# Performance work log

Hardware: AMD Instinct MI355X
Metric: run time of the kernel (lower is better)

The kernel has to match this reference:

```python
import jax, jax.numpy as jnp
import numpy as np

B, S, C, H = 2, 2048, 1024, 16
D = C // H  # depth per head = 64


def mish(x):
    return x * jnp.tanh(jax.nn.softplus(x))


def setup_inputs() -> dict:
    key = jax.random.key(0)
    ks = jax.random.split(key, 11)
    s = 1.0 / np.sqrt(C)
    return {
        "x": jax.random.normal(ks[0], (B, S, C), jnp.float32),
        "y": jax.random.normal(ks[1], (B, S, C), jnp.float32),
        "t_mat": jax.random.normal(ks[2], (B, S, S), jnp.float32),
        "wq": jax.random.normal(ks[3], (C, C), jnp.float32) * s,
        "bq": jnp.zeros((C,), jnp.float32),
        "wk": jax.random.normal(ks[4], (C, C), jnp.float32) * s,
        "bk": jnp.zeros((C,), jnp.float32),
        "wv": jax.random.normal(ks[5], (C, C), jnp.float32) * s,
        "bv": jnp.zeros((C,), jnp.float32),
        "wc": jax.random.normal(ks[6], (H,), jnp.float32),   # 1x1 Conv2D, 1 in-channel -> H out-channels
        "bc": jnp.zeros((H,), jnp.float32),
        "wf": jax.random.normal(ks[7], (C, C), jnp.float32) * s,  # 1x1 Conv1D == per-position Dense
        "bf": jnp.zeros((C,), jnp.float32),
    }


def _split_heads(t):
    # (B, S, C) -> (B*H, S, D)
    return t.reshape(B, S, H, D).transpose(0, 2, 1, 3).reshape(B * H, S, D)


def reference(x, y, t_mat, wq, bq, wk, bk, wv, bv, wc, bc, wf, bf):
    q = _split_heads(y @ wq + bq)   # (BH, S, D)
    k = _split_heads(x @ wk + bk)
    v = _split_heads(y @ wv + bv)

    # context: 1x1 conv + tanh over t_mat -> (B, S, S, H) -> (B*H, S, S)
    c = jnp.tanh(t_mat[..., None] * wc + bc)
    c = c.transpose(0, 3, 1, 2).reshape(B * H, S, S)

    qk = jnp.einsum("bkd,bqd->bkq", k, q) / jnp.sqrt(jnp.float32(D))  # (BH, Sk, Sq)
    cv = jnp.einsum("bks,bsd->bkd", c, v)                             # (BH, S, D)
    att = jnp.einsum("bkq,bqd->bkd", qk, cv)                          # (BH, S, D)

    # merge heads: (BH, S, D) -> (B, S, C)
    merged = att.reshape(B, H, S, D).transpose(0, 2, 1, 3).reshape(B, S, C)
    return mish(merged @ wf + bf)
```

## Files before the change

### kernel.cpp

```cpp
#include <hip/hip_runtime.h>
#include <math.h>

#define B_ 2
#define S_ 2048
#define C_ 1024
#define H_ 16
#define D_ 64

typedef __bf16 bf16_t;
typedef __attribute__((ext_vector_type(8))) __bf16 bf16x8;
typedef __attribute__((ext_vector_type(4))) __bf16 bf16x4;
typedef __attribute__((ext_vector_type(4))) float f32x4;

__device__ __forceinline__ void gload16(const void* g, void* l) {
    __builtin_amdgcn_global_load_lds(
        (const __attribute__((address_space(1))) unsigned int*)g,
        (__attribute__((address_space(3))) unsigned int*)l, 16, 0, 0);
}

__device__ __forceinline__ float tanh_fast(float z) {
    z = fminf(fmaxf(z, -12.f), 12.f);
    float e = __expf(2.f * z);
    return 1.f - __fdividef(2.f, e + 1.f);
}

__device__ __forceinline__ float mish_f(float x) {
    float sp = (x > 15.f) ? x : log1pf(__expf(x));
    return x * tanh_fast(sp);
}

__device__ __forceinline__ float tanh_folded(float t, float w2, float b2) {
    float e = __builtin_amdgcn_exp2f(fmaf(t, w2, b2));
    float r = __builtin_amdgcn_rcpf(e + 1.f);
    return fmaf(-2.f, r, 1.f);
}

__global__ __launch_bounds__(256) void prep_kernel(
    const float* __restrict__ y, bf16_t* __restrict__ ybf,
    const float* __restrict__ x, bf16_t* __restrict__ xbf,
    const float* __restrict__ wq, const float* __restrict__ wk,
    const float* __restrict__ wv,
    bf16_t* __restrict__ wqt, bf16_t* __restrict__ wkt,
    bf16_t* __restrict__ wvt)
{
    __shared__ float ts[64][65];
    const int bid = blockIdx.x;
    const int t = threadIdx.x;
    if (bid < 4096) {
        const float* in = (bid < 2048) ? y : x;
        bf16_t* out = (bid < 2048) ? ybf : xbf;
        size_t i = ((size_t)(bid & 2047) * 256 + t) * 8;
        float4 u = *(const float4*)&in[i];
        float4 v = *(const float4*)&in[i + 4];
        bf16x8 o;
        o[0] = (bf16_t)u.x; o[1] = (bf16_t)u.y; o[2] = (bf16_t)u.z; o[3] = (bf16_t)u.w;
        o[4] = (bf16_t)v.x; o[5] = (bf16_t)v.y; o[6] = (bf16_t)v.z; o[7] = (bf16_t)v.w;
        *(bf16x8*)&out[i] = o;
    } else {
        const int r3 = bid - 4096;
        const int z = r3 >> 8;
        const int rem = r3 & 255;
        const int k0 = (rem >> 4) * 64, n0 = (rem & 15) * 64;
        const float* in = z == 0 ? wq : (z == 1 ? wk : wv);
        bf16_t* out = z == 0 ? wqt : (z == 1 ? wkt : wvt);
        const int r = t >> 2, c0 = (t & 3) * 16;
        #pragma unroll
        for (int j = 0; j < 16; j += 4) {
            float4 v = *(const float4*)&in[(size_t)(k0 + r) * C_ + n0 + c0 + j];
            ts[c0 + j + 0][r] = v.x; ts[c0 + j + 1][r] = v.y;
            ts[c0 + j + 2][r] = v.z; ts[c0 + j + 3][r] = v.w;
        }
        __syncthreads();
        #pragma unroll
        for (int g = 0; g < 2; ++g) {
            bf16x8 o;
            #pragma unroll
            for (int e = 0; e < 8; ++e) o[e] = (bf16_t)ts[r][c0 + g * 8 + e];
            *(bf16x8*)&out[(size_t)(n0 + r) * C_ + k0 + c0 + g * 8] = o;
        }
    }
}

__global__ __launch_bounds__(256) void qkv_proj(
    const bf16_t* __restrict__ ybf, const bf16_t* __restrict__ xbf,
    const bf16_t* __restrict__ wqt, const bf16_t* __restrict__ wkt,
    const bf16_t* __restrict__ wvt,
    const float* __restrict__ bq, const float* __restrict__ bk,
    const float* __restrict__ bv,
    bf16_t* __restrict__ Qt, bf16_t* __restrict__ Kb, bf16_t* __restrict__ Vt)
{
    const int z = blockIdx.z;
    const bf16_t* A  = (z == 1) ? xbf : ybf;
    const bf16_t* Bt = (z == 0) ? wqt : (z == 1) ? wkt : wvt;
    const float* bias = (z == 0) ? bq : (z == 1) ? bk : bv;
    const int K = C_;

    __shared__ bf16_t As[128 * 32];
    __shared__ bf16_t Bs[128 * 32];

    const int t = threadIdx.x;
    const int w = t >> 6, lane = t & 63;
    const int wm = (w >> 1) * 64, wn = (w & 1) * 64;
    const int l15 = lane & 15, l4 = lane >> 4;
    const int row0 = blockIdx.y * 128, col0 = blockIdx.x * 128;

    const int sr = t >> 2, sk = (t & 3) * 8;
    const bf16_t* gA = A + (size_t)(row0 + sr) * K + sk;
    const bf16_t* gB = Bt + (size_t)(col0 + sr) * K + sk;
    bf16_t* lA = As + (t & ~63) * 8;
    bf16_t* lB = Bs + (t & ~63) * 8;

    f32x4 acc[4][4] = {};

    for (int k0 = 0; k0 < K; k0 += 32) {
        __syncthreads();
        gload16(gA + k0, lA);
        gload16(gA + k0 + (size_t)64 * K, lA + 2048);
        gload16(gB + k0, lB);
        gload16(gB + k0 + (size_t)64 * K, lB + 2048);
        __syncthreads();
        bf16x8 a[4], b[4];
        #pragma unroll
        for (int i = 0; i < 4; ++i)
            a[i] = *(const bf16x8*)&As[(wm + i * 16 + l15) * 32 + l4 * 8];
        #pragma unroll
        for (int j = 0; j < 4; ++j)
            b[j] = *(const bf16x8*)&Bs[(wn + j * 16 + l15) * 32 + l4 * 8];
        #pragma unroll
        for (int i = 0; i < 4; ++i)
            #pragma unroll
            for (int j = 0; j < 4; ++j)
                acc[i][j] = __builtin_amdgcn_mfma_f32_16x16x32_bf16(
                    a[i], b[j], acc[i][j], 0, 0, 0);
    }

    if (z != 1) {
        bf16_t* To = (z == 0) ? Qt : Vt;
        #pragma unroll
        for (int i = 0; i < 4; ++i) {
            int mb = row0 + wm + i * 16 + l4 * 4;
            int b2 = mb >> 11, s = mb & 2047;
            #pragma unroll
            for (int j = 0; j < 4; ++j) {
                int c = col0 + wn + j * 16 + l15;
                float bv2 = bias[c];
                bf16x4 o;
                #pragma unroll
                for (int r = 0; r < 4; ++r) o[r] = (bf16_t)(acc[i][j][r] + bv2);
                *(bf16x4*)&To[((size_t)b2 * C_ + c) * S_ + s] = o;
            }
        }
    } else {
        #pragma unroll
        for (int i = 0; i < 4; ++i)
            #pragma unroll
            for (int j = 0; j < 4; ++j) {
                int c = col0 + wn + j * 16 + l15;
                float bv2 = bias[c];
                #pragma unroll
                for (int r = 0; r < 4; ++r) {
                    int m = row0 + wm + i * 16 + l4 * 4 + r;
                    Kb[(size_t)m * C_ + c] = (bf16_t)(acc[i][j][r] + bv2);
                }
            }
    }
}

__global__ __launch_bounds__(256) void cv_qtcv_fused(
    const float* __restrict__ t_mat, const bf16_t* __restrict__ Vt,
    const bf16_t* __restrict__ Qt,
    const float* __restrict__ wc, const float* __restrict__ bc,
    float* __restrict__ Mm)
{
    const int bh = blockIdx.z, b = bh >> 4, h = bh & 15;
    const int q0 = blockIdx.x * 128;
    const int p = blockIdx.y;
    const int t = threadIdx.x;
    const int w = t >> 6, lane = t & 63;
    const int l15 = lane & 15, l4 = lane >> 4;

    __shared__ bf16_t smem[10240];
    bf16_t* As = smem;
    bf16_t* Bs = smem + 4096;
    bf16_t* cvs = smem;

    const float LOG2E2 = 2.8853900817779268f;
    const float wch2 = wc[h] * LOG2E2, bch2 = bc[h] * LOG2E2;
    const float* tb = t_mat + (size_t)b * S_ * S_ + (size_t)q0 * S_;
    const bf16_t* Vb = Vt + ((size_t)b * C_ + h * 64) * S_;

    const int rr = t >> 1, sp = (t & 1) * 16;
    const int vd = t >> 2, vse = (t & 3) * 8;
    const int lBoff = (t & ~63) * 8;

    f32x4 acc[2][4] = {};

    const int s_beg = p * 512, s_end = s_beg + 512;
    const float* trow = tb + (size_t)rr * S_ + sp;

    float4 v0 = *(const float4*)&trow[s_beg];
    float4 v1 = *(const float4*)&trow[s_beg + 4];
    float4 v2 = *(const float4*)&trow[s_beg + 8];
    float4 v3 = *(const float4*)&trow[s_beg + 12];

    int buf = 0;
    for (int s0 = s_beg; s0 < s_end; s0 += 32, buf ^= 1) {
        bf16x8 p0, p1;
        p0[0] = (bf16_t)tanh_folded(v0.x, wch2, bch2);
        p0[1] = (bf16_t)tanh_folded(v0.y, wch2, bch2);
        p0[2] = (bf16_t)tanh_folded(v0.z, wch2, bch2);
        p0[3] = (bf16_t)tanh_folded(v0.w, wch2, bch2);
        p0[4] = (bf16_t)tanh_folded(v1.x, wch2, bch2);
        p0[5] = (bf16_t)tanh_folded(v1.y, wch2, bch2);
        p0[6] = (bf16_t)tanh_folded(v1.z, wch2, bch2);
        p0[7] = (bf16_t)tanh_folded(v1.w, wch2, bch2);
        p1[0] = (bf16_t)tanh_folded(v2.x, wch2, bch2);
        p1[1] = (bf16_t)tanh_folded(v2.y, wch2, bch2);
        p1[2] = (bf16_t)tanh_folded(v2.z, wch2, bch2);
        p1[3] = (bf16_t)tanh_folded(v2.w, wch2, bch2);
        p1[4] = (bf16_t)tanh_folded(v3.x, wch2, bch2);
        p1[5] = (bf16_t)tanh_folded(v3.y, wch2, bch2);
        p1[6] = (bf16_t)tanh_folded(v3.z, wch2, bch2);
        p1[7] = (bf16_t)tanh_folded(v3.w, wch2, bch2);
        gload16(Vb + (size_t)vd * S_ + s0 + vse, Bs + buf * 2048 + lBoff);
        *(bf16x8*)&As[rr * 32 + sp] = p0;
        *(bf16x8*)&As[rr * 32 + sp + 8] = p1;
        __syncthreads();
        if (s0 + 32 < s_end) {
            const float* nrow = &trow[s0 + 32];
            v0 = *(const float4*)&nrow[0];
            v1 = *(const float4*)&nrow[4];
            v2 = *(const float4*)&nrow[8];
            v3 = *(const float4*)&nrow[12];
        }
        bf16x8 a0 = *(const bf16x8*)&As[(w * 32 + l15) * 32 + l4 * 8];
        bf16x8 a1 = *(const bf16x8*)&As[(w * 32 + 16 + l15) * 32 + l4 * 8];
        #pragma unroll
        for (int j = 0; j < 4; ++j) {
            bf16x8 bb = *(const bf16x8*)&Bs[buf * 2048 + (j * 16 + l15) * 32 + l4 * 8];
            acc[0][j] = __builtin_amdgcn_mfma_f32_16x16x32_bf16(a0, bb, acc[0][j], 0, 0, 0);
            acc[1][j] = __builtin_amdgcn_mfma_f32_16x16x32_bf16(a1, bb, acc[1][j], 0, 0, 0);
        }
    }

    __syncthreads();
    #pragma unroll
    for (int i = 0; i < 2; ++i)
        #pragma unroll
        for (int j = 0; j < 4; ++j) {
            int d = j * 16 + l15;
            bf16x4 o;
            #pragma unroll
            for (int r = 0; r < 4; ++r) o[r] = (bf16_t)acc[i][j][r];
            *(bf16x4*)&cvs[(size_t)w * 2560 + d * 40 + i * 16 + l4 * 4] = o;
        }
    __syncthreads();

    const bf16_t* Qrow = Qt + ((size_t)b * C_ + h * 64 + w * 16 + l15) * S_ + q0 + l4 * 8;
    f32x4 macc[4] = {};
    #pragma unroll
    for (int c = 0; c < 4; ++c) {
        bf16x8 a = *(const bf16x8*)&Qrow[c * 32];
        #pragma unroll
        for (int j = 0; j < 4; ++j) {
            bf16x8 bb = *(const bf16x8*)&cvs[(size_t)c * 2560 + (j * 16 + l15) * 40 + l4 * 8];
            macc[j] = __builtin_amdgcn_mfma_f32_16x16x32_bf16(a, bb, macc[j], 0, 0, 0);
        }
    }

    float* mp = Mm + (size_t)bh * 64 * 64;
    #pragma unroll
    for (int j = 0; j < 4; ++j)
        #pragma unroll
        for (int r = 0; r < 4; ++r)
            atomicAdd(&mp[(size_t)(w * 16 + l4 * 4 + r) * 64 + j * 16 + l15],
                      macc[j][r]);
}

__global__ __launch_bounds__(256) void weff_kernel(
    const float* __restrict__ Mm, const float* __restrict__ wf,
    bf16_t* __restrict__ Wefft)
{
    const int b = blockIdx.z, h = blockIdx.y;
    const int co0 = blockIdx.x * 64;
    const int t = threadIdx.x;
    const int tx = t & 15, ty = t >> 4;

    __shared__ float Ms[64][64];
    __shared__ float Ws[64][64];

    const float* Mb = Mm + (size_t)(b * H_ + h) * 64 * 64;

    const int r  = t >> 2;
    const int c4 = (t & 3) << 2;

    #pragma unroll
    for (int rep = 0; rep < 4; ++rep) {
        int col = c4 + rep * 16;
        float4 m4 = *(const float4*)&Mb[(size_t)r * 64 + col];
        Ms[col + 0][r] = m4.x; Ms[col + 1][r] = m4.y;
        Ms[col + 2][r] = m4.z; Ms[col + 3][r] = m4.w;
        float4 w4 = *(const float4*)&wf[(size_t)(h * 64 + r) * C_ + co0 + col];
        *(float4*)&Ws[r][col] = w4;
    }
    __syncthreads();

    float acc[4][4] = {};
    #pragma unroll
    for (int kk = 0; kk < 64; ++kk) {
        float av[4], bv2[4];
        *(float4*)&av[0] = *(const float4*)&Ms[kk][ty * 4];
        *(float4*)&bv2[0] = *(const float4*)&Ws[kk][tx * 4];
        #pragma unroll
        for (int i = 0; i < 4; ++i)
            #pragma unroll
            for (int j = 0; j < 4; ++j)
                acc[i][j] = fmaf(av[i], bv2[j], acc[i][j]);
    }

    bf16_t* wp = Wefft + (size_t)b * C_ * C_;
    #pragma unroll
    for (int i = 0; i < 4; ++i)
        #pragma unroll
        for (int j = 0; j < 4; ++j)
            wp[(size_t)(co0 + tx * 4 + j) * C_ + h * 64 + ty * 4 + i] =
                (bf16_t)(acc[i][j] * 0.125f);
}

__global__ __launch_bounds__(256) void final_gemm(
    const bf16_t* __restrict__ Kb, const bf16_t* __restrict__ Weft,
    const float* __restrict__ bias, float* __restrict__ out)
{
    const int z = blockIdx.z;
    const bf16_t* A  = Kb + (size_t)z * S_ * C_;
    const bf16_t* Bt = Weft + (size_t)z * C_ * C_;
    float* Co = out + (size_t)z * S_ * C_;
    const int K = C_;

    __shared__ bf16_t As[128 * 32];
    __shared__ bf16_t Bs[64 * 32];

    const int t = threadIdx.x;
    const int w = t >> 6, lane = t & 63;
    const int l15 = lane & 15, l4 = lane >> 4;
    const int row0 = blockIdx.y * 128, col0 = blockIdx.x * 64;

    const int sr = t >> 2, sk = (t & 3) * 8;
    const bf16_t* gA = A + (size_t)(row0 + sr) * K + sk;
    const bf16_t* gB = Bt + (size_t)(col0 + sr) * K + sk;
    bf16_t* lA = As + (t & ~63) * 8;
    bf16_t* lB = Bs + (t & ~63) * 8;

    f32x4 acc[2][4] = {};

    for (int k0 = 0; k0 < K; k0 += 32) {
        __syncthreads();
        gload16(gA + k0, lA);
        gload16(gA + k0 + (size_t)64 * K, lA + 2048);
        gload16(gB + k0, lB);
        __syncthreads();
        bf16x8 a0 = *(const bf16x8*)&As[(w * 32 + l15) * 32 + l4 * 8];
        bf16x8 a1 = *(const bf16x8*)&As[(w * 32 + 16 + l15) * 32 + l4 * 8];
        #pragma unroll
        for (int j = 0; j < 4; ++j) {
            bf16x8 bb = *(const bf16x8*)&Bs[(j * 16 + l15) * 32 + l4 * 8];
            acc[0][j] = __builtin_amdgcn_mfma_f32_16x16x32_bf16(a0, bb, acc[0][j], 0, 0, 0);
            acc[1][j] = __builtin_amdgcn_mfma_f32_16x16x32_bf16(a1, bb, acc[1][j], 0, 0, 0);
        }
    }

    #pragma unroll
    for (int i = 0; i < 2; ++i)
        #pragma unroll
        for (int j = 0; j < 4; ++j) {
            int c = col0 + j * 16 + l15;
            float bv2 = bias[c];
            #pragma unroll
            for (int r = 0; r < 4; ++r) {
                int m = row0 + w * 32 + i * 16 + l4 * 4 + r;
                Co[(size_t)m * C_ + c] = mish_f(acc[i][j][r] + bv2);
            }
        }
}

extern "C" void kernel_launch(void* const* d_in, const int* in_sizes, int n_in,
                              void* d_out, int out_size, void* d_ws, size_t ws_size,
                              hipStream_t stream) {
    const float* x     = (const float*)d_in[0];
    const float* y     = (const float*)d_in[1];
    const float* t_mat = (const float*)d_in[2];
    const float* wq    = (const float*)d_in[3];
    const float* bq    = (const float*)d_in[4];
    const float* wk    = (const float*)d_in[5];
    const float* bk    = (const float*)d_in[6];
    const float* wv    = (const float*)d_in[7];
    const float* bv    = (const float*)d_in[8];
    const float* wc    = (const float*)d_in[9];
    const float* bc    = (const float*)d_in[10];
    const float* wf    = (const float*)d_in[11];
    const float* bf    = (const float*)d_in[12];
    float* out = (float*)d_out;

    char* base = (char*)d_ws;
    bf16_t* Qt   = (bf16_t*)(base + 0);
    bf16_t* Kb   = (bf16_t*)(base + 8388608);
    bf16_t* Vt   = (bf16_t*)(base + 16777216);
    float*  Mm   = (float*) (base + 25165824);
    bf16_t* Weft = (bf16_t*)(base + 25690112);
    bf16_t* ybf  = (bf16_t*)(base + 29884416);
    bf16_t* xbf  = (bf16_t*)(base + 38273024);
    bf16_t* wqt  = (bf16_t*)(base + 46661632);
    bf16_t* wkt  = (bf16_t*)(base + 48758784);
    bf16_t* wvt  = (bf16_t*)(base + 50855936);

    hipMemsetAsync(Mm, 0, (size_t)B_ * H_ * 64 * 64 * sizeof(float), stream);

    dim3 blk(256);

    prep_kernel<<<dim3(4864), blk, 0, stream>>>(
        y, ybf, x, xbf, wq, wk, wv, wqt, wkt, wvt);

    qkv_proj<<<dim3(C_ / 128, (B_ * S_) / 128, 3), blk, 0, stream>>>(
        ybf, xbf, wqt, wkt, wvt, bq, bk, bv, Qt, Kb, Vt);

    cv_qtcv_fused<<<dim3(S_ / 128, 4, B_ * H_), blk, 0, stream>>>(
        t_mat, Vt, Qt, wc, bc, Mm);

    weff_kernel<<<dim3(C_ / 64, H_, B_), blk, 0, stream>>>(Mm, wf, Weft);

    final_gemm<<<dim3(C_ / 64, S_ / 128, B_), blk, 0, stream>>>(
        Kb, Weft, bf, out);
}
```

Baseline: 274.1 us.

## Process two heads per block in fused cv kernel to reuse t_mat loads

Each block of the fused context-value kernel now handles a pair of heads, so every t_mat tile loaded from global memory feeds two tanh transforms and two MFMA accumulations. This halves the t_mat reads, which dominate memory traffic (t_mat is read once per head). In exchange there is twice the accumulator registers, more LDS (32KB), half as many blocks, and the Q·cv epilogue runs serially for both heads.

```diff
diff --git a/kernel.cpp b/kernel.cpp
--- a/kernel.cpp
+++ b/kernel.cpp
@@ -33,6 +33,19 @@
     float e = __builtin_amdgcn_exp2f(fmaf(t, w2, b2));
     float r = __builtin_amdgcn_rcpf(e + 1.f);
     return fmaf(-2.f, r, 1.f);
+}
+
+__device__ __forceinline__ bf16x8 tanh8(float4 u, float4 v, float w2, float b2) {
+    bf16x8 o;
+    o[0] = (bf16_t)tanh_folded(u.x, w2, b2);
+    o[1] = (bf16_t)tanh_folded(u.y, w2, b2);
+    o[2] = (bf16_t)tanh_folded(u.z, w2, b2);
+    o[3] = (bf16_t)tanh_folded(u.w, w2, b2);
+    o[4] = (bf16_t)tanh_folded(v.x, w2, b2);
+    o[5] = (bf16_t)tanh_folded(v.y, w2, b2);
+    o[6] = (bf16_t)tanh_folded(v.z, w2, b2);
+    o[7] = (bf16_t)tanh_folded(v.w, w2, b2);
+    return o;
 }
 
 __global__ __launch_bounds__(256) void prep_kernel(
@@ -172,28 +185,34 @@
     const float* __restrict__ wc, const float* __restrict__ bc,
     float* __restrict__ Mm)
 {
-    const int bh = blockIdx.z, b = bh >> 4, h = bh & 15;
+    const int bhp = blockIdx.z;
+    const int b = bhp >> 3, hp = bhp & 7;
+    const int h0 = hp * 2, h1 = h0 + 1;
     const int q0 = blockIdx.x * 128;
     const int p = blockIdx.y;
     const int t = threadIdx.x;
     const int w = t >> 6, lane = t & 63;
     const int l15 = lane & 15, l4 = lane >> 4;
 
-    __shared__ bf16_t smem[10240];
-    bf16_t* As = smem;
-    bf16_t* Bs = smem + 4096;
+    __shared__ bf16_t smem[16384];
+    bf16_t* As0 = smem;
+    bf16_t* As1 = smem + 4096;
+    bf16_t* Bsb = smem + 8192;
     bf16_t* cvs = smem;
 
     const float LOG2E2 = 2.8853900817779268f;
-    const float wch2 = wc[h] * LOG2E2, bch2 = bc[h] * LOG2E2;
+    const float w20 = wc[h0] * LOG2E2, b20 = bc[h0] * LOG2E2;
+    const float w21 = wc[h1] * LOG2E2, b21 = bc[h1] * LOG2E2;
     const float* tb = t_mat + (size_t)b * S_ * S_ + (size_t)q0 * S_;
-    const bf16_t* Vb = Vt + ((size_t)b * C_ + h * 64) * S_;
+    const bf16_t* Vb0 = Vt + ((size_t)b * C_ + h0 * 64) * S_;
+    const bf16_t* Vb1 = Vb0 + (size_t)64 * S_;
 
     const int rr = t >> 1, sp = (t & 1) * 16;
     const int vd = t >> 2, vse = (t & 3) * 8;
     const int lBoff = (t & ~63) * 8;
 
-    f32x4 acc[2][4] = {};
+    f32x4 acc0[2][4] = {};
+    f32x4 acc1[2][4] = {};
 
     const int s_beg = p * 512, s_end = s_beg + 512;
     const float* trow = tb + (size_t)rr * S_ + sp;
@@ -205,26 +224,16 @@
 
     int buf = 0;
     for (int s0 = s_beg; s0 < s_end; s0 += 32, buf ^= 1) {
-        bf16x8 p0, p1;
-        p0[0] = (bf16_t)tanh_folded(v0.x, wch2, bch2);
-        p0[1] = (bf16_t)tanh_folded(v0.y, wch2, bch2);
-        p0[2] = (bf16_t)tanh_folded(v0.z, wch2, bch2);
-        p0[3] = (bf16_t)tanh_folded(v0.w, wch2, bch2);
-        p0[4] = (bf16_t)tanh_folded(v1.x, wch2, bch2);
-        p0[5] = (bf16_t)tanh_folded(v1.y, wch2, bch2);
-        p0[6] = (bf16_t)tanh_folded(v1.z, wch2, bch2);
-        p0[7] = (bf16_t)tanh_folded(v1.w, wch2, bch2);
-        p1[0] = (bf16_t)tanh_folded(v2.x, wch2, bch2);
-        p1[1] = (bf16_t)tanh_folded(v2.y, wch2, bch2);
-        p1[2] = (bf16_t)tanh_folded(v2.z, wch2, bch2);
-        p1[3] = (bf16_t)tanh_folded(v2.w, wch2, bch2);
-        p1[4] = (bf16_t)tanh_folded(v3.x, wch2, bch2);
-        p1[5] = (bf16_t)tanh_folded(v3.y, wch2, bch2);
-        p1[6] = (bf16_t)tanh_folded(v3.z, wch2, bch2);
-        p1[7] = (bf16_t)tanh_folded(v3.w, wch2, bch2);
-        gload16(Vb + (size_t)vd * S_ + s0 + vse, Bs + buf * 2048 + lBoff);
-        *(bf16x8*)&As[rr * 32 + sp] = p0;
-        *(bf16x8*)&As[rr * 32 + sp + 8] = p1;
+        gload16(Vb0 + (size_t)vd * S_ + s0 + vse, Bsb + (0 + buf) * 2048 + lBoff);
+        gload16(Vb1 + (size_t)vd * S_ + s0 + vse, Bsb + (2 + buf) * 2048 + lBoff);
+        bf16x8 p00 = tanh8(v0, v1, w20, b20);
+        bf16x8 p01 = tanh8(v2, v3, w20, b20);
+        bf16x8 p10 = tanh8(v0, v1, w21, b21);
+        bf16x8 p11 = tanh8(v2, v3, w21, b21);
+        *(bf16x8*)&As0[rr * 32 + sp]     = p00;
+        *(bf16x8*)&As0[rr * 32 + sp + 8] = p01;
+        *(bf16x8*)&As1[rr * 32 + sp]     = p10;
+        *(bf16x8*)&As1[rr * 32 + sp + 8] = p11;
         __syncthreads();
         if (s0 + 32 < s_end) {
             const float* nrow = &trow[s0 + 32];
@@ -233,48 +242,63 @@
             v2 = *(const float4*)&nrow[8];
             v3 = *(const float4*)&nrow[12];
         }
-        bf16x8 a0 = *(const bf16x8*)&As[(w * 32 + l15) * 32 + l4 * 8];
-        bf16x8 a1 = *(const bf16x8*)&As[(w * 32 + 16 + l15) * 32 + l4 * 8];
+        bf16x8 a0 = *(const bf16x8*)&As0[(w * 32 + l15) * 32 + l4 * 8];
+        bf16x8 a1 = *(const bf16x8*)&As0[(w * 32 + 16 + l15) * 32 + l4 * 8];
         #pragma unroll
         for (int j = 0; j < 4; ++j) {
-            bf16x8 bb = *(const bf16x8*)&Bs[buf * 2048 + (j * 16 + l15) * 32 + l4 * 8];
-            acc[0][j] = __builtin_amdgcn_mfma_f32_16x16x32_bf16(a0, bb, acc[0][j], 0, 0, 0);
-            acc[1][j] = __builtin_amdgcn_mfma_f32_16x16x32_bf16(a1, bb, acc[1][j], 0, 0, 0);
-        }
-    }
-
-    __syncthreads();
+            bf16x8 bb = *(const bf16x8*)&Bsb[(0 + buf) * 2048 + (j * 16 + l15) * 32 + l4 * 8];
+            acc0[0][j] = __builtin_amdgcn_mfma_f32_16x16x32_bf16(a0, bb, acc0[0][j], 0, 0, 0);
+            acc0[1][j] = __builtin_amdgcn_mfma_f32_16x16x32_bf16(a1, bb, acc0[1][j], 0, 0, 0);
+        }
+        bf16x8 c0 = *(const bf16x8*)&As1[(w * 32 + l15) * 32 + l4 * 8];
+        bf16x8 c1 = *(const bf16x8*)&As1[(w * 32 + 16 + l15) * 32 + l4 * 8];
+        #pragma unroll
+        for (int j = 0; j < 4; ++j) {
+            bf16x8 bb = *(const bf16x8*)&Bsb[(2 + buf) * 2048 + (j * 16 + l15) * 32 + l4 * 8];
+            acc1[0][j] = __builtin_amdgcn_mfma_f32_16x16x32_bf16(c0, bb, acc1[0][j], 0, 0, 0);
+            acc1[1][j] = __builtin_amdgcn_mfma_f32_16x16x32_bf16(c1, bb, acc1[1][j], 0, 0, 0);
+        }
+    }
+
     #pragma unroll
-    for (int i = 0; i < 2; ++i)
-        #pragma unroll
-        for (int j = 0; j < 4; ++j) {
-            int d = j * 16 + l15;
-            bf16x4 o;
-            #pragma unroll
-            for (int r = 0; r < 4; ++r) o[r] = (bf16_t)acc[i][j][r];
-            *(bf16x4*)&cvs[(size_t)w * 2560 + d * 40 + i * 16 + l4 * 4] = o;
-        }
-    __syncthreads();
-
-    const bf16_t* Qrow = Qt + ((size_t)b * C_ + h * 64 + w * 16 + l15) * S_ + q0 + l4 * 8;
-    f32x4 macc[4] = {};
-    #pragma unroll
-    for (int c = 0; c < 4; ++c) {
-        bf16x8 a = *(const bf16x8*)&Qrow[c * 32];
-        #pragma unroll
-        for (int j = 0; j < 4; ++j) {
-            bf16x8 bb = *(const bf16x8*)&cvs[(size_t)c * 2560 + (j * 16 + l15) * 40 + l4 * 8];
-            macc[j] = __builtin_amdgcn_mfma_f32_16x16x32_bf16(a, bb, macc[j], 0, 0, 0);
-        }
-    }
-
-    float* mp = Mm + (size_t)bh * 64 * 64;
-    #pragma unroll
-    for (int j = 0; j < 4; ++j)
-        #pragma unroll
-        for (int r = 0; r < 4; ++r)
-            atomicAdd(&mp[(size_t)(w * 16 + l4 * 4 + r) * 64 + j * 16 + l15],
-                      macc[j][r]);
+    for (int g = 0; g < 2; ++g) {
+        const int h = g ? h1 : h0;
+        __syncthreads();
+        #pragma unroll
+        for (int i = 0; i < 2; ++i)
+            #pragma unroll
+            for (int j = 0; j < 4; ++j) {
+                int d = j * 16 + l15;
+                bf16x4 o;
+                #pragma unroll
+                for (int r = 0; r < 4; ++r)
+                    o[r] = (bf16_t)(g ? acc1[i][j][r] : acc0[i][j][r]);
+                *(bf16x4*)&cvs[(size_t)w * 2560 + d * 40 + i * 16 + l4 * 4] = o;
+            }
+        __syncthreads();
+
+        const bf16_t* Qrow = Qt + ((size_t)b * C_ + h * 64 + w * 16 + l15) * S_
+                             + q0 + l4 * 8;
+        f32x4 macc[4] = {};
+        #pragma unroll
+        for (int c = 0; c < 4; ++c) {
+            bf16x8 a = *(const bf16x8*)&Qrow[c * 32];
+            #pragma unroll
+            for (int j = 0; j < 4; ++j) {
+                bf16x8 bb = *(const bf16x8*)&cvs[(size_t)c * 2560 +
+                                                 (j * 16 + l15) * 40 + l4 * 8];
+                macc[j] = __builtin_amdgcn_mfma_f32_16x16x32_bf16(a, bb, macc[j], 0, 0, 0);
+            }
+        }
+
+        float* mp = Mm + (size_t)(b * H_ + h) * 64 * 64;
+        #pragma unroll
+        for (int j = 0; j < 4; ++j)
+            #pragma unroll
+            for (int r = 0; r < 4; ++r)
+                atomicAdd(&mp[(size_t)(w * 16 + l4 * 4 + r) * 64 + j * 16 + l15],
+                          macc[j][r]);
+    }
 }
 
 __global__ __launch_bounds__(256) void weff_kernel(
@@ -423,7 +447,7 @@
     qkv_proj<<<dim3(C_ / 128, (B_ * S_) / 128, 3), blk, 0, stream>>>(
         ybf, xbf, wqt, wkt, wvt, bq, bk, bv, Qt, Kb, Vt);
 
-    cv_qtcv_fused<<<dim3(S_ / 128, 4, B_ * H_), blk, 0, stream>>>(
+    cv_qtcv_fused<<<dim3(S_ / 128, 4, B_ * H_ / 2), blk, 0, stream>>>(
         t_mat, Vt, Qt, wc, bc, Mm);
 
     weff_kernel<<<dim3(C_ / 64, H_, B_), blk, 0, stream>>>(Mm, wf, Weft);
```

Result: slower. 282.3 us (+3.0%).
